# Optimization experiments

Hardware: AMD Instinct MI355X
Metric: run time of the kernel (lower is better)

The kernel has to match this reference:

```python
import jax, jax.numpy as jnp
import numpy as np

D_MODEL = 1024
HEAD = 16
D_K = D_MODEL // HEAD
NEG_INF = -1.0e9


def setup_inputs() -> dict:
    key = jax.random.key(0)
    ks = jax.random.split(key, 12)
    B, S = 2, 2048
    scale = 1.0 / np.sqrt(D_MODEL)
    inp = {
        "query": jax.random.normal(ks[0], (B, S, D_MODEL), jnp.float32),
        "key": jax.random.normal(ks[1], (B, S, D_MODEL), jnp.float32),
        "value": jax.random.normal(ks[2], (B, S, D_MODEL), jnp.float32),
        "mask": jax.random.randint(ks[3], (B, 1, 1, S), 0, 2, jnp.int32),
        "Wq": jax.random.normal(ks[4], (D_MODEL, D_MODEL), jnp.float32) * scale,
        "bq": jnp.zeros((D_MODEL,), jnp.float32),
        "Wk": jax.random.normal(ks[5], (D_MODEL, D_MODEL), jnp.float32) * scale,
        "bk": jnp.zeros((D_MODEL,), jnp.float32),
        "Wv": jax.random.normal(ks[6], (D_MODEL, D_MODEL), jnp.float32) * scale,
        "bv": jnp.zeros((D_MODEL,), jnp.float32),
        "Wo": jax.random.normal(ks[7], (D_MODEL, D_MODEL), jnp.float32) * scale,
        "bo": jnp.zeros((D_MODEL,), jnp.float32),
    }
    return inp


def reference(query, key, value, mask, Wq, bq, Wk, bk, Wv, bv, Wo, bo):
    B, S, _ = query.shape
    # QKV projections (torch nn.Linear: x @ W^T + b)
    q = query @ Wq.T + bq
    k = key @ Wk.T + bk
    v = value @ Wv.T + bv
    # [B, H, S, d_k]
    q = q.reshape(B, S, HEAD, D_K).transpose(0, 2, 1, 3)
    k = k.reshape(B, S, HEAD, D_K).transpose(0, 2, 1, 3)
    v = v.reshape(B, S, HEAD, D_K).transpose(0, 2, 1, 3)
    # scores [B, H, S, S]
    scores = jnp.einsum("bhqd,bhkd->bhqk", q, k) / jnp.sqrt(jnp.float32(D_K))
    scores = jnp.where(mask == 0, jnp.float32(NEG_INF), scores)
    attn = jax.nn.softmax(scores, axis=-1)  # dropout off (eval mode)
    ctx = jnp.einsum("bhqk,bhkd->bhqd", attn, v)
    ctx = ctx.transpose(0, 2, 1, 3).reshape(B, S, D_MODEL)
    return ctx @ Wo.T + bo
```

## Files before the change

### kernel.cpp

```cpp
#include <hip/hip_runtime.h>
#include <cstdint>
#include <cstddef>

typedef unsigned short u16;
typedef unsigned int   u32;
typedef __bf16 bf16x8 __attribute__((ext_vector_type(8)));
typedef float  f32x4  __attribute__((ext_vector_type(4)));

#define D_MODEL 1024
#define SEQ     2048
#define NTOK    4096
#define NHEAD   16
#define DK      64

#define FENCE() asm volatile("" ::: "memory")
#define SBAR()  asm volatile("s_barrier" ::: "memory")
#define WVL(N)  asm volatile("s_waitcnt vmcnt(" #N ") lgkmcnt(0)" ::: "memory")

__device__ __forceinline__ float fast_exp2(float x) {
  return __builtin_amdgcn_exp2f(x);
}

__device__ __forceinline__ u16 f2bf(float f) {
  u32 u = __builtin_bit_cast(u32, f);
  u += 0x7fffu + ((u >> 16) & 1u);
  return (u16)(u >> 16);
}

__device__ __forceinline__ u32 pkbf(float a, float b) {
  u16 x = __builtin_bit_cast(u16, (__bf16)a);
  u16 y = __builtin_bit_cast(u16, (__bf16)b);
  return (u32)x | ((u32)y << 16);
}

__device__ __forceinline__ void gload16(const u16* g, u16* l) {
  __builtin_amdgcn_global_load_lds(
      (__attribute__((address_space(1))) void*)(uintptr_t)g,
      (__attribute__((address_space(3))) void*)l,
      16, 0, 0);
}

__global__ __launch_bounds__(256) void mask_scan(const int* __restrict__ mask,
                                                 int* __restrict__ idx,
                                                 int* __restrict__ cnt) {
  const int b = blockIdx.x, t = threadIdx.x;
  const int lane = t & 63, w = t >> 6;
  __shared__ int sW[4];
  __shared__ int sTot;
  int m8[8];
  const int base = b * SEQ + t * 8;
  int tot = 0;
#pragma unroll
  for (int i = 0; i < 8; ++i) {
    m8[i] = (mask[base + i] != 0);
    tot += m8[i];
  }
  int v = tot;
#pragma unroll
  for (int d = 1; d < 64; d <<= 1) {
    int u = __shfl_up(v, d);
    if (lane >= d) v += u;
  }
  if (lane == 63) sW[w] = v;
  __syncthreads();
  if (t == 0) {
    int run = 0;
#pragma unroll
    for (int i = 0; i < 4; ++i) { int tmp = sW[i]; sW[i] = run; run += tmp; }
    sTot = run;
  }
  __syncthreads();
  int pos = v - tot + sW[w];
#pragma unroll
  for (int i = 0; i < 8; ++i)
    if (m8[i]) idx[b * SEQ + pos++] = t * 8 + i;
  const int cn = sTot;
  if (t == 0) cnt[b] = cn;
  for (int j = cn + t; j < SEQ; j += 256) idx[b * SEQ + j] = 0;
}

__global__ __launch_bounds__(256) void w_convert(
    const float* __restrict__ wq, const float* __restrict__ wk,
    const float* __restrict__ wv, const float* __restrict__ wo,
    u16* __restrict__ wb) {
  const int total = 1 << 20;
  for (int cid = blockIdx.x * blockDim.x + threadIdx.x; cid < total;
       cid += gridDim.x * blockDim.x) {
    int which = cid >> 18;
    int off = cid & ((1 << 18) - 1);
    const float* src = which == 0 ? wq : (which == 1 ? wk : (which == 2 ? wv : wo));
    u16* dst = wb + ((size_t)which << 20);
    float4 f = ((const float4*)src)[off];
    ushort4 u;
    u.x = f2bf(f.x); u.y = f2bf(f.y); u.z = f2bf(f.z); u.w = f2bf(f.w);
    ((ushort4*)dst)[off] = u;
  }
}

__global__ __launch_bounds__(256, 3) void gemm_qkv(
    const float* __restrict__ Aq, const float* __restrict__ Ak,
    const float* __restrict__ Av, const u16* __restrict__ Bw,
    const float* __restrict__ b0, const float* __restrict__ b1,
    const float* __restrict__ b2, u16* __restrict__ Cout) {
  __shared__ __align__(16) u16 smem[3 * 128 * 64];
  u16* sA = smem;

  const int t = threadIdx.x;
  const int z = blockIdx.z;
  const float* Ap = (z == 0) ? Aq : ((z == 1) ? Ak : Av);
  const u16* Bp = Bw + ((size_t)z << 20);
  const float* bias = (z == 0) ? b0 : ((z == 1) ? b1 : b2);
  const float scl = (z == 0) ? 0.18033688011f : 1.0f;

  const int m0 = blockIdx.x * 128, n0 = blockIdx.y * 128;
  const int lane = t & 63, wv = t >> 6;
  const int wm = (wv >> 1) * 64, wn = (wv & 1) * 64;
  const int c = lane & 15, qd = lane >> 4;

  const int arow = t >> 3;
  const int aoff = (((t & 7) - arow) & 7) * 8;
  const float* gaA = Ap + (size_t)(m0 + arow) * D_MODEL + aoff;
  const u16* gaB = Bp + (size_t)(n0 + arow) * D_MODEL + aoff;

  float4 pa[4][2];
  u32 cv[4][4];

#pragma unroll
  for (int j = 0; j < 4; ++j) {
    pa[j][0] = *(const float4*)(gaA + (size_t)(32 * j) * D_MODEL);
    pa[j][1] = *(const float4*)(gaA + (size_t)(32 * j) * D_MODEL + 4);
  }
  FENCE();
#pragma unroll
  for (int j = 0; j < 4; ++j)
    gload16(gaB + (size_t)(32 * j) * D_MODEL, smem + 8192 + (t + 256 * j) * 8);
  WVL(4);
#pragma unroll
  for (int j = 0; j < 4; ++j) {
    cv[j][0] = pkbf(pa[j][0].x, pa[j][0].y);
    cv[j][1] = pkbf(pa[j][0].z, pa[j][0].w);
    cv[j][2] = pkbf(pa[j][1].x, pa[j][1].y);
    cv[j][3] = pkbf(pa[j][1].z, pa[j][1].w);
  }
  FENCE();
#pragma unroll
  for (int j = 0; j < 4; ++j) {
    pa[j][0] = *(const float4*)(gaA + 64 + (size_t)(32 * j) * D_MODEL);
    pa[j][1] = *(const float4*)(gaA + 64 + (size_t)(32 * j) * D_MODEL + 4);
  }
  FENCE();
#pragma unroll
  for (int j = 0; j < 4; ++j) {
    uint4 v4 = {cv[j][0], cv[j][1], cv[j][2], cv[j][3]};
    *(uint4*)&sA[(t + 256 * j) * 8] = v4;
  }

  f32x4 acc[4][4] = {};

#pragma unroll
  for (int kbi = 0; kbi < 16; ++kbi) {
    const int cur = kbi & 1;
    if (kbi == 15) { WVL(0); } else { WVL(8); }
    SBAR();
    if (kbi + 1 < 16) {
      u16* sBn = smem + 8192 + (1 - cur) * 8192;
      const int kb2 = (kbi + 1) * 64;
#pragma unroll
      for (int j = 0; j < 4; ++j)
        gload16(gaB + kb2 + (size_t)(32 * j) * D_MODEL, sBn + (t + 256 * j) * 8);
    }
    FENCE();
    const u16* sB = smem + 8192 + cur * 8192;
#pragma unroll
    for (int s = 0; s < 2; ++s) {
      const int ao = ((s * 4 + qd + wm + c) & 7) * 8;
      const int bo = ((s * 4 + qd + wn + c) & 7) * 8;
      bf16x8 af[4], bfr[4];
#pragma unroll
      for (int i = 0; i < 4; ++i)
        af[i] = *(const bf16x8*)&sA[(wm + i * 16 + c) * 64 + ao];
#pragma unroll
      for (int j = 0; j < 4; ++j)
        bfr[j] = *(const bf16x8*)&sB[(wn + j * 16 + c) * 64 + bo];
#pragma unroll
      for (int i = 0; i < 4; ++i)
#pragma unroll
        for (int j = 0; j < 4; ++j)
          acc[i][j] = __builtin_amdgcn_mfma_f32_16x16x32_bf16(af[i], bfr[j],
                                                              acc[i][j], 0, 0, 0);
    }
    if (kbi + 1 < 16) {
      WVL(4);
#pragma unroll
      for (int j = 0; j < 4; ++j) {
        cv[j][0] = pkbf(pa[j][0].x, pa[j][0].y);
        cv[j][1] = pkbf(pa[j][0].z, pa[j][0].w);
        cv[j][2] = pkbf(pa[j][1].x, pa[j][1].y);
        cv[j][3] = pkbf(pa[j][1].z, pa[j][1].w);
      }
      if (kbi + 2 < 16) {
        const int kb3 = (kbi + 2) * 64;
#pragma unroll
        for (int j = 0; j < 4; ++j) {
          pa[j][0] = *(const float4*)(gaA + kb3 + (size_t)(32 * j) * D_MODEL);
          pa[j][1] = *(const float4*)(gaA + kb3 + (size_t)(32 * j) * D_MODEL + 4);
        }
      }
      FENCE();
      SBAR();
#pragma unroll
      for (int j = 0; j < 4; ++j) {
        uint4 v4 = {cv[j][0], cv[j][1], cv[j][2], cv[j][3]};
        *(uint4*)&sA[(t + 256 * j) * 8] = v4;
      }
    }
  }
  __syncthreads();

  u16* sC = smem;
  if (z == 2) {
#pragma unroll
    for (int j = 0; j < 4; ++j) {
      const int col = wn + j * 16 + c;
      const float bv = bias[n0 + col];
#pragma unroll
      for (int i = 0; i < 4; ++i)
#pragma unroll
        for (int r = 0; r < 4; ++r)
          sC[col * 136 + wm + i * 16 + qd * 4 + r] = f2bf(acc[i][j][r] + bv);
    }
    __syncthreads();
    u16* VT = Cout + ((size_t)2 << 22);
    const int bb = m0 >> 11, s0 = m0 & 2047;
    const int sidx = (t & 15) * 8;
#pragma unroll
    for (int outer = 0; outer < 8; ++outer) {
      const int vrow = outer * 16 + (t >> 4);
      const int col = n0 + vrow;
      const int hh = col >> 6, dd = col & 63;
      uint4 val = *(const uint4*)&sC[vrow * 136 + sidx];
      *(uint4*)&VT[((size_t)((bb * NHEAD + hh) * DK + dd)) * SEQ + s0 + sidx] =
          val;
    }
  } else {
#pragma unroll
    for (int j = 0; j < 4; ++j) {
      const int col = wn + j * 16 + c;
      const float bv = bias[n0 + col];
#pragma unroll
      for (int i = 0; i < 4; ++i)
#pragma unroll
        for (int r = 0; r < 4; ++r)
          sC[(wm + i * 16 + qd * 4 + r) * 136 + col] =
              f2bf((acc[i][j][r] + bv) * scl);
    }
    __syncthreads();
    u16* outp = Cout + ((size_t)z << 22);
    const int cidx = (t & 15) * 8;
#pragma unroll
    for (int outer = 0; outer < 8; ++outer) {
      const int lrow = outer * 16 + (t >> 4);
      uint4 val = *(const uint4*)&sC[lrow * 136 + cidx];
      *(uint4*)&outp[(size_t)(m0 + lrow) * D_MODEL + n0 + cidx] = val;
    }
  }
}

__global__ __launch_bounds__(256) void vtc_gather(const u16* __restrict__ VT,
                                                  const int* __restrict__ idx,
                                                  const int* __restrict__ cnt,
                                                  u16* __restrict__ VTc) {
  const int row = blockIdx.x;
  const int b = row >> 10;
  const int cn = cnt[b];
  const u16* src = VT + (size_t)row * SEQ;
  u16* dst = VTc + (size_t)row * SEQ;
  const int* ib = idx + b * SEQ;
  for (int j = threadIdx.x; j < cn; j += 256) dst[j] = src[ib[j]];
}

__global__ __launch_bounds__(256) void mha_attn(
    const u16* __restrict__ QKVb, const u16* __restrict__ VTc,
    const int* __restrict__ idx, const int* __restrict__ cnt,
    u16* __restrict__ Opart, float* __restrict__ ml) {
  __shared__ __align__(16) u16 sK[64 * 72];
  __shared__ __align__(16) u16 sVt[64 * 72];
  __shared__ __align__(16) u16 sP[128 * 72];

  const int t = threadIdx.x, lane = t & 63, wq = t >> 6;
  const int c = lane & 15, qd = lane >> 4;
  const int qb = blockIdx.x, h = blockIdx.y;
  const int b = blockIdx.z & 1, ck = blockIdx.z >> 1;

  const int cn = cnt[b];
  const int nb = (cn + 63) >> 6;
  const int half = (nb + 1) >> 1;
  const int kstart = ck ? half : 0;
  const int kend = ck ? nb : half;

  const u16* Qg = QKVb;
  const u16* Kg = QKVb + ((size_t)4 << 20);
  const u16* VTch = VTc + ((size_t)((b * NHEAD + h) * DK)) * SEQ;
  const int rowbase = b * SEQ;
  const int colbase = h * DK;

  bf16x8 aq[2][2];
#pragma unroll
  for (int qt = 0; qt < 2; ++qt) {
    const u16* g = Qg +
                   (size_t)(rowbase + qb * 128 + wq * 32 + qt * 16 + c) * D_MODEL +
                   colbase + qd * 8;
    aq[qt][0] = *(const bf16x8*)g;
    aq[qt][1] = *(const bf16x8*)(g + 32);
  }

  float l[2] = {0.f, 0.f};
  f32x4 o[2][4] = {};
  const float MADD = -1.4426950e9f;
  const float MFIX = 16.0f;

  const int r0s = t >> 2, offs = (t & 3) * 16;
  const u16* gvb = VTch + (size_t)r0s * SEQ + offs;
  const int* idxb = idx + b * SEQ + r0s;

  uint4 k0, k1, v0, v1;
  int sNext2 = 0;
  if (kstart < kend) {
    const int s0i = idxb[kstart * 64];
    const u16* gk = Kg + (size_t)(rowbase + s0i) * D_MODEL + colbase + offs;
    const u16* gv = gvb + kstart * 64;
    k0 = *(const uint4*)gk;
    k1 = *(const uint4*)(gk + 8);
    v0 = *(const uint4*)gv;
    v1 = *(const uint4*)(gv + 8);
    if (kstart + 1 < kend) sNext2 = idxb[(kstart + 1) * 64];
  }

  for (int kbi = kstart; kbi < kend; ++kbi) {
    __syncthreads();
    *(uint4*)&sK[r0s * 72 + offs] = k0;
    *(uint4*)&sK[r0s * 72 + offs + 8] = k1;
    *(uint4*)&sVt[r0s * 72 + offs] = v0;
    *(uint4*)&sVt[r0s * 72 + offs + 8] = v1;
    __syncthreads();
    if (kbi + 1 < kend) {
      const u16* gk = Kg + (size_t)(rowbase + sNext2) * D_MODEL + colbase + offs;
      const u16* gv = gvb + (kbi + 1) * 64;
      k0 = *(const uint4*)gk;
      k1 = *(const uint4*)(gk + 8);
      v0 = *(const uint4*)gv;
      v1 = *(const uint4*)(gv + 8);
    }
    if (kbi + 2 < kend) sNext2 = idxb[(kbi + 2) * 64];

    const bool full = ((kbi + 1) << 6) <= cn;
    f32x4 st[2][4];
#pragma unroll
    for (int tt = 0; tt < 4; ++tt) {
      bf16x8 ak0 = *(const bf16x8*)&sK[(tt * 16 + c) * 72 + qd * 8];
      bf16x8 ak1 = *(const bf16x8*)&sK[(tt * 16 + c) * 72 + qd * 8 + 32];
      f32x4 cin;
      if (full) {
        cin = f32x4{0.f, 0.f, 0.f, 0.f};
      } else {
        const int jb = (kbi << 6) + tt * 16 + qd * 4;
        cin = f32x4{jb + 0 < cn ? 0.f : MADD, jb + 1 < cn ? 0.f : MADD,
                    jb + 2 < cn ? 0.f : MADD, jb + 3 < cn ? 0.f : MADD};
      }
#pragma unroll
      for (int qt = 0; qt < 2; ++qt) {
        f32x4 a =
            __builtin_amdgcn_mfma_f32_16x16x32_bf16(ak0, aq[qt][0], cin, 0, 0, 0);
        a = __builtin_amdgcn_mfma_f32_16x16x32_bf16(ak1, aq[qt][1], a, 0, 0, 0);
        st[qt][tt] = a;
      }
    }

#pragma unroll
    for (int qt = 0; qt < 2; ++qt) {
      float sum = 0.f;
      const int prow = (wq * 32 + qt * 16 + c) * 72;
#pragma unroll
      for (int tt = 0; tt < 4; ++tt) {
        u32 pk[2];
#pragma unroll
        for (int pr = 0; pr < 2; ++pr) {
          u32 p0 = __builtin_bit_cast(u32, fast_exp2(st[qt][tt][2 * pr] - MFIX));
          u32 p1 =
              __builtin_bit_cast(u32, fast_exp2(st[qt][tt][2 * pr + 1] - MFIX));
          u32 hi1 = p1 & 0xffff0000u;
          pk[pr] = (p0 >> 16) | hi1;
          sum += __builtin_bit_cast(float, p0 & 0xffff0000u);
          sum += __builtin_bit_cast(float, hi1);
        }
        uint2 pv2 = {pk[0], pk[1]};
        *(uint2*)&sP[prow + tt * 16 + qd * 4] = pv2;
      }
      l[qt] += sum;
    }

    bf16x8 bp[2][2];
#pragma unroll
    for (int qt = 0; qt < 2; ++qt) {
      const int prow = (wq * 32 + qt * 16 + c) * 72;
      bp[qt][0] = *(const bf16x8*)&sP[prow + qd * 8];
      bp[qt][1] = *(const bf16x8*)&sP[prow + qd * 8 + 32];
    }
#pragma unroll
    for (int dt = 0; dt < 4; ++dt) {
      bf16x8 av0 = *(const bf16x8*)&sVt[(dt * 16 + c) * 72 + qd * 8];
      bf16x8 av1 = *(const bf16x8*)&sVt[(dt * 16 + c) * 72 + qd * 8 + 32];
#pragma unroll
      for (int qt = 0; qt < 2; ++qt) {
        o[qt][dt] =
            __builtin_amdgcn_mfma_f32_16x16x32_bf16(av0, bp[qt][0], o[qt][dt], 0, 0, 0);
        o[qt][dt] =
            __builtin_amdgcn_mfma_f32_16x16x32_bf16(av1, bp[qt][1], o[qt][dt], 0, 0, 0);
      }
    }
  }

  const size_t obase =
      (size_t)ck * 4194304 + ((size_t)((b * NHEAD + h) * SEQ) + qb * 128) * 64;
  const int mlbase = ((ck * 2 + b) * NHEAD + h) * SEQ + qb * 128;
#pragma unroll
  for (int qt = 0; qt < 2; ++qt) {
    float ls = l[qt];
    ls += __shfl_xor(ls, 16);
    ls += __shfl_xor(ls, 32);
    const float inv = (ls != 0.f) ? 1.0f / ls : 0.f;
    const int q = wq * 32 + qt * 16 + c;
#pragma unroll
    for (int dt = 0; dt < 4; ++dt) {
      u32 lo = (u32)f2bf(o[qt][dt][0] * inv) |
               ((u32)f2bf(o[qt][dt][1] * inv) << 16);
      u32 hi = (u32)f2bf(o[qt][dt][2] * inv) |
               ((u32)f2bf(o[qt][dt][3] * inv) << 16);
      uint2 ov = {lo, hi};
      *(uint2*)&Opart[obase + (size_t)q * 64 + dt * 16 + qd * 4] = ov;
    }
    if (qd == 0) ml[mlbase + q] = ls;
  }
}

__global__ __launch_bounds__(256) void mha_combine(
    const u16* __restrict__ Opart, const float* __restrict__ ml,
    u16* __restrict__ ctx) {
  const int tid = blockIdx.x * 256 + threadIdx.x;
  const int row = tid >> 3, d0 = (tid & 7) * 8;
  const int b = row >> 15, h = (row >> 11) & 15, q = row & 2047;
  float l1 = ml[row];
  float l2 = ml[65536 + row];
  float inv = 1.0f / (l1 + l2);
  float w1 = l1 * inv, w2 = l2 * inv;
  const size_t o1 = (size_t)row * 64 + d0;
  uint4 pa = *(const uint4*)(Opart + o1);
  uint4 pb = *(const uint4*)(Opart + 4194304 + o1);
  u32 wa[4] = {pa.x, pa.y, pa.z, pa.w};
  u32 wb[4] = {pb.x, pb.y, pb.z, pb.w};
  u32 out[4];
#pragma unroll
  for (int j = 0; j < 4; ++j) {
    float alo = __builtin_bit_cast(float, wa[j] << 16);
    float ahi = __builtin_bit_cast(float, wa[j] & 0xffff0000u);
    float blo = __builtin_bit_cast(float, wb[j] << 16);
    float bhi = __builtin_bit_cast(float, wb[j] & 0xffff0000u);
    float rlo = w1 * alo + w2 * blo;
    float rhi = w1 * ahi + w2 * bhi;
    out[j] = (u32)f2bf(rlo) | ((u32)f2bf(rhi) << 16);
  }
  uint4 ov = {out[0], out[1], out[2], out[3]};
  *(uint4*)&ctx[((size_t)(b * SEQ + q)) * D_MODEL + h * DK + d0] = ov;
}

__global__ __launch_bounds__(256) void gemm_out(
    const u16* __restrict__ A, const u16* __restrict__ Bw,
    const float* __restrict__ bias, float* __restrict__ Cout) {
  __shared__ __align__(16) u16 sAb[2][128 * 64];
  __shared__ __align__(16) u16 sBc[2][64 * 64];

  const int t = threadIdx.x;
  const int m0 = blockIdx.x * 128, n0 = blockIdx.y * 64;
  const int lane = t & 63, wv = t >> 6;
  const int wm = (wv >> 1) * 64, wn = (wv & 1) * 32;
  const int c = lane & 15, qd = lane >> 4;

  const int arow = t >> 3;
  const int aoff = (((t & 7) - arow) & 7) * 8;
  const u16* gaA = A + (size_t)(m0 + arow) * D_MODEL + aoff;
  const u16* gaB = Bw + (size_t)(n0 + arow) * D_MODEL + aoff;

#pragma unroll
  for (int j = 0; j < 4; ++j)
    gload16(gaA + (size_t)(32 * j) * D_MODEL, &sAb[0][(t + 256 * j) * 8]);
#pragma unroll
  for (int j = 0; j < 2; ++j)
    gload16(gaB + (size_t)(32 * j) * D_MODEL, &sBc[0][(t + 256 * j) * 8]);

  f32x4 acc[4][2] = {};

  for (int kbi = 0; kbi < 16; ++kbi) {
    const int cur = kbi & 1;
    __syncthreads();
    if (kbi + 1 < 16) {
      const int kb2 = (kbi + 1) * 64;
#pragma unroll
      for (int j = 0; j < 4; ++j)
        gload16(gaA + kb2 + (size_t)(32 * j) * D_MODEL,
                &sAb[1 - cur][(t + 256 * j) * 8]);
#pragma unroll
      for (int j = 0; j < 2; ++j)
        gload16(gaB + kb2 + (size_t)(32 * j) * D_MODEL,
                &sBc[1 - cur][(t + 256 * j) * 8]);
    }
    const u16* sA = sAb[cur];
    const u16* sB = sBc[cur];
#pragma unroll
    for (int s = 0; s < 2; ++s) {
      const int ao = ((s * 4 + qd + wm + c) & 7) * 8;
      const int bo = ((s * 4 + qd + wn + c) & 7) * 8;
      bf16x8 af[4], bfr[2];
#pragma unroll
      for (int i = 0; i < 4; ++i)
        af[i] = *(const bf16x8*)&sA[(wm + i * 16 + c) * 64 + ao];
#pragma unroll
      for (int j = 0; j < 2; ++j)
        bfr[j] = *(const bf16x8*)&sB[(wn + j * 16 + c) * 64 + bo];
#pragma unroll
      for (int i = 0; i < 4; ++i)
#pragma unroll
        for (int j = 0; j < 2; ++j)
          acc[i][j] = __builtin_amdgcn_mfma_f32_16x16x32_bf16(af[i], bfr[j],
                                                              acc[i][j], 0, 0, 0);
    }
  }

#pragma unroll
  for (int j = 0; j < 2; ++j) {
    const int col = n0 + wn + j * 16 + c;
    const float bv = bias[col];
#pragma unroll
    for (int i = 0; i < 4; ++i)
#pragma unroll
      for (int r = 0; r < 4; ++r) {
        const int row = m0 + wm + i * 16 + qd * 4 + r;
        Cout[(size_t)row * D_MODEL + col] = acc[i][j][r] + bv;
      }
  }
}

extern "C" void kernel_launch(void* const* d_in, const int* in_sizes, int n_in,
                              void* d_out, int out_size, void* d_ws,
                              size_t ws_size, hipStream_t stream) {
  const float* query = (const float*)d_in[0];
  const float* key   = (const float*)d_in[1];
  const float* value = (const float*)d_in[2];
  const int*   mask  = (const int*)d_in[3];
  const float* Wq = (const float*)d_in[4];
  const float* bq = (const float*)d_in[5];
  const float* Wk = (const float*)d_in[6];
  const float* bk = (const float*)d_in[7];
  const float* Wv = (const float*)d_in[8];
  const float* bv = (const float*)d_in[9];
  const float* Wo = (const float*)d_in[10];
  const float* bo = (const float*)d_in[11];

  u16* ws  = (u16*)d_ws;
  u16* Wb  = ws + ((size_t)12 << 20);
  u16* QKV = ws + ((size_t)16 << 20);
  u16* CTX = ws + ((size_t)28 << 20);
  u16* VTc = ws;
  u16* Opart = ws + ((size_t)4 << 20);
  float* ml = (float*)(ws + ((size_t)12 << 20));
  int* idxp = (int*)(ws + ((size_t)28 << 20));
  int* cntp = idxp + 2 * SEQ;

  mask_scan<<<dim3(2), dim3(256), 0, stream>>>(mask, idxp, cntp);
  w_convert<<<dim3(1024), dim3(256), 0, stream>>>(Wq, Wk, Wv, Wo, Wb);
  gemm_qkv<<<dim3(32, 8, 3), dim3(256), 0, stream>>>(query, key, value, Wb, bq,
                                                     bk, bv, QKV);
  vtc_gather<<<dim3(2048), dim3(256), 0, stream>>>(QKV + ((size_t)8 << 20), idxp,
                                                   cntp, VTc);
  mha_attn<<<dim3(16, 16, 4), dim3(256), 0, stream>>>(QKV, VTc, idxp, cntp,
                                                      Opart, ml);
  mha_combine<<<dim3(2048), dim3(256), 0, stream>>>(Opart, ml, CTX);
  gemm_out<<<dim3(32, 16), dim3(256), 0, stream>>>(CTX, Wb + ((size_t)3 << 20),
                                                   bo, (float*)d_out);
}
```

Before: 214.2 us.

## Load QKV GEMM A operand directly into MFMA registers, bypassing LDS

In the QKV projection GEMM, each wave now loads its fp32 A-tile fragments straight from global memory in MFMA layout and converts them to bf16 in registers. The A staging through shared memory, its extra barrier and the LDS reads are removed, and shared memory shrinks to just the B double buffer. In exchange, each wave reads A independently, so A rows are fetched twice across the wave pair and load coalescing is narrower. Global latency is hidden only by a half-step register prefetch, and the vmcnt accounting gets trickier.

```diff
diff --git a/kernel.cpp b/kernel.cpp
--- a/kernel.cpp
+++ b/kernel.cpp
@@ -102,8 +102,7 @@
     const float* __restrict__ Av, const u16* __restrict__ Bw,
     const float* __restrict__ b0, const float* __restrict__ b1,
     const float* __restrict__ b2, u16* __restrict__ Cout) {
-  __shared__ __align__(16) u16 smem[3 * 128 * 64];
-  u16* sA = smem;
+  __shared__ __align__(16) u16 smem[128 * 136];
 
   const int t = threadIdx.x;
   const int z = blockIdx.z;
@@ -119,66 +118,60 @@
 
   const int arow = t >> 3;
   const int aoff = (((t & 7) - arow) & 7) * 8;
-  const float* gaA = Ap + (size_t)(m0 + arow) * D_MODEL + aoff;
   const u16* gaB = Bp + (size_t)(n0 + arow) * D_MODEL + aoff;
 
-  float4 pa[4][2];
-  u32 cv[4][4];
-
-#pragma unroll
-  for (int j = 0; j < 4; ++j) {
-    pa[j][0] = *(const float4*)(gaA + (size_t)(32 * j) * D_MODEL);
-    pa[j][1] = *(const float4*)(gaA + (size_t)(32 * j) * D_MODEL + 4);
-  }
+  const float* gA = Ap + (size_t)(m0 + wm + c) * D_MODEL + qd * 8;
+
+  float4 paN[4][2];
+
+#pragma unroll
+  for (int j = 0; j < 4; ++j)
+    gload16(gaB + (size_t)(32 * j) * D_MODEL, smem + (t + 256 * j) * 8);
   FENCE();
 #pragma unroll
-  for (int j = 0; j < 4; ++j)
-    gload16(gaB + (size_t)(32 * j) * D_MODEL, smem + 8192 + (t + 256 * j) * 8);
-  WVL(4);
-#pragma unroll
-  for (int j = 0; j < 4; ++j) {
-    cv[j][0] = pkbf(pa[j][0].x, pa[j][0].y);
-    cv[j][1] = pkbf(pa[j][0].z, pa[j][0].w);
-    cv[j][2] = pkbf(pa[j][1].x, pa[j][1].y);
-    cv[j][3] = pkbf(pa[j][1].z, pa[j][1].w);
+  for (int i = 0; i < 4; ++i) {
+    paN[i][0] = *(const float4*)(gA + (size_t)(16 * i) * D_MODEL);
+    paN[i][1] = *(const float4*)(gA + (size_t)(16 * i) * D_MODEL + 4);
   }
   FENCE();
-#pragma unroll
-  for (int j = 0; j < 4; ++j) {
-    pa[j][0] = *(const float4*)(gaA + 64 + (size_t)(32 * j) * D_MODEL);
-    pa[j][1] = *(const float4*)(gaA + 64 + (size_t)(32 * j) * D_MODEL + 4);
-  }
-  FENCE();
-#pragma unroll
-  for (int j = 0; j < 4; ++j) {
-    uint4 v4 = {cv[j][0], cv[j][1], cv[j][2], cv[j][3]};
-    *(uint4*)&sA[(t + 256 * j) * 8] = v4;
-  }
 
   f32x4 acc[4][4] = {};
 
 #pragma unroll
   for (int kbi = 0; kbi < 16; ++kbi) {
     const int cur = kbi & 1;
-    if (kbi == 15) { WVL(0); } else { WVL(8); }
+    const u16* sB = smem + cur * 8192;
+    u16* sBn = smem + (1 - cur) * 8192;
+    const int kb = kbi * 64;
+
+    WVL(8);
     SBAR();
+    WVL(0);
+
+    bf16x8 af[4];
+#pragma unroll
+    for (int i = 0; i < 4; ++i) {
+      uint4 v4 = {pkbf(paN[i][0].x, paN[i][0].y), pkbf(paN[i][0].z, paN[i][0].w),
+                  pkbf(paN[i][1].x, paN[i][1].y), pkbf(paN[i][1].z, paN[i][1].w)};
+      af[i] = __builtin_bit_cast(bf16x8, v4);
+    }
+    FENCE();
+#pragma unroll
+    for (int i = 0; i < 4; ++i) {
+      paN[i][0] = *(const float4*)(gA + kb + 32 + (size_t)(16 * i) * D_MODEL);
+      paN[i][1] = *(const float4*)(gA + kb + 36 + (size_t)(16 * i) * D_MODEL);
+    }
+    FENCE();
     if (kbi + 1 < 16) {
-      u16* sBn = smem + 8192 + (1 - cur) * 8192;
-      const int kb2 = (kbi + 1) * 64;
 #pragma unroll
       for (int j = 0; j < 4; ++j)
-        gload16(gaB + kb2 + (size_t)(32 * j) * D_MODEL, sBn + (t + 256 * j) * 8);
+        gload16(gaB + kb + 64 + (size_t)(32 * j) * D_MODEL,
+                sBn + (t + 256 * j) * 8);
     }
     FENCE();
-    const u16* sB = smem + 8192 + cur * 8192;
-#pragma unroll
-    for (int s = 0; s < 2; ++s) {
-      const int ao = ((s * 4 + qd + wm + c) & 7) * 8;
-      const int bo = ((s * 4 + qd + wn + c) & 7) * 8;
-      bf16x8 af[4], bfr[4];
-#pragma unroll
-      for (int i = 0; i < 4; ++i)
-        af[i] = *(const bf16x8*)&sA[(wm + i * 16 + c) * 64 + ao];
+    {
+      const int bo = ((qd + wn + c) & 7) * 8;
+      bf16x8 bfr[4];
 #pragma unroll
       for (int j = 0; j < 4; ++j)
         bfr[j] = *(const bf16x8*)&sB[(wn + j * 16 + c) * 64 + bo];
@@ -189,30 +182,34 @@
           acc[i][j] = __builtin_amdgcn_mfma_f32_16x16x32_bf16(af[i], bfr[j],
                                                               acc[i][j], 0, 0, 0);
     }
+    if (kbi + 1 < 16) { WVL(4); } else { WVL(0); }
+#pragma unroll
+    for (int i = 0; i < 4; ++i) {
+      uint4 v4 = {pkbf(paN[i][0].x, paN[i][0].y), pkbf(paN[i][0].z, paN[i][0].w),
+                  pkbf(paN[i][1].x, paN[i][1].y), pkbf(paN[i][1].z, paN[i][1].w)};
+      af[i] = __builtin_bit_cast(bf16x8, v4);
+    }
+    FENCE();
     if (kbi + 1 < 16) {
-      WVL(4);
-#pragma unroll
-      for (int j = 0; j < 4; ++j) {
-        cv[j][0] = pkbf(pa[j][0].x, pa[j][0].y);
-        cv[j][1] = pkbf(pa[j][0].z, pa[j][0].w);
-        cv[j][2] = pkbf(pa[j][1].x, pa[j][1].y);
-        cv[j][3] = pkbf(pa[j][1].z, pa[j][1].w);
+#pragma unroll
+      for (int i = 0; i < 4; ++i) {
+        paN[i][0] = *(const float4*)(gA + kb + 64 + (size_t)(16 * i) * D_MODEL);
+        paN[i][1] = *(const float4*)(gA + kb + 68 + (size_t)(16 * i) * D_MODEL);
       }
-      if (kbi + 2 < 16) {
-        const int kb3 = (kbi + 2) * 64;
-#pragma unroll
-        for (int j = 0; j < 4; ++j) {
-          pa[j][0] = *(const float4*)(gaA + kb3 + (size_t)(32 * j) * D_MODEL);
-          pa[j][1] = *(const float4*)(gaA + kb3 + (size_t)(32 * j) * D_MODEL + 4);
-        }
-      }
-      FENCE();
-      SBAR();
-#pragma unroll
-      for (int j = 0; j < 4; ++j) {
-        uint4 v4 = {cv[j][0], cv[j][1], cv[j][2], cv[j][3]};
-        *(uint4*)&sA[(t + 256 * j) * 8] = v4;
-      }
+    }
+    FENCE();
+    {
+      const int bo = ((4 + qd + wn + c) & 7) * 8;
+      bf16x8 bfr[4];
+#pragma unroll
+      for (int j = 0; j < 4; ++j)
+        bfr[j] = *(const bf16x8*)&sB[(wn + j * 16 + c) * 64 + bo];
+#pragma unroll
+      for (int i = 0; i < 4; ++i)
+#pragma unroll
+        for (int j = 0; j < 4; ++j)
+          acc[i][j] = __builtin_amdgcn_mfma_f32_16x16x32_bf16(af[i], bfr[j],
+                                                              acc[i][j], 0, 0, 0);
     }
   }
   __syncthreads();
```

Result: slower. 269.7 us (+25.9%).
